# Performance work log

Measured on AMD Instinct MI355X. Metric: run time of the kernel, lower is better.

## Reference

```python
import jax, jax.numpy as jnp
import numpy as np

B, L, E, H = 8, 2048, 768, 512

def setup_inputs() -> dict:
    key = jax.random.key(0)
    ks = jax.random.split(key, 12)
    s = 0.05
    rn = lambda k, shp: jax.random.normal(k, shp, dtype=jnp.float32) * s
    return {
        "embedded_inputs": jax.random.normal(ks[0], (B, L, E), dtype=jnp.float32),
        "decoder_input_init": jax.random.normal(ks[1], (B, H), dtype=jnp.float32),
        "W_ih": rn(ks[2], (4 * H, E)), "W_hh": rn(ks[3], (4 * H, H)),
        "b_ih": jnp.zeros((4 * H,), jnp.float32), "b_hh": jnp.zeros((4 * H,), jnp.float32),
        "Wd_in": rn(ks[4], (4 * H, H)), "bd_in": jnp.zeros((4 * H,), jnp.float32),
        "Wd_hh": rn(ks[5], (4 * H, H)), "bd_hh": jnp.zeros((4 * H,), jnp.float32),
        "W_inp": rn(ks[6], (H, H)), "b_inp": jnp.zeros((H,), jnp.float32),
        "Wc": rn(ks[7], (H, H)), "bc": jnp.zeros((H,), jnp.float32),
        "V": jax.random.uniform(ks[8], (H,), minval=-1.0, maxval=1.0, dtype=jnp.float32),
        "W_out": rn(ks[9], (H, 2 * H)), "b_out": jnp.zeros((H,), jnp.float32),
    }


def _lstm_cell(x, h, c, W_in, b_in, W_hid, b_hid):
    # gates chunked in (input, forget, cell, out) order, matching torch .chunk(4,1)
    g = x @ W_in.T + b_in + h @ W_hid.T + b_hid
    i, f, gc, o = jnp.split(g, 4, axis=-1)
    c_t = jax.nn.sigmoid(f) * c + jax.nn.sigmoid(i) * jnp.tanh(gc)
    h_t = jax.nn.sigmoid(o) * jnp.tanh(c_t)
    return h_t, c_t


def _encode(x, W_ih, W_hh, b_ih, b_hh):
    # x: [B, L, E] -> outputs [B, L, H], last (h, c)
    Hh = W_hh.shape[1]
    h0 = jnp.zeros((x.shape[0], Hh), x.dtype)
    def step(carry, xt):
        h, c = carry
        h, c = _lstm_cell(xt, h, c, W_ih, b_ih, W_hh, b_hh)
        return (h, c), h
    (hT, cT), outs = jax.lax.scan(step, (h0, h0), x.transpose(1, 0, 2))
    return outs.transpose(1, 0, 2), hT, cT


def reference(embedded_inputs, decoder_input_init, W_ih, W_hh, b_ih, b_hh,
              Wd_in, bd_in, Wd_hh, bd_hh, W_inp, b_inp, Wc, bc, V, W_out, b_out):
    enc_out, h, c = _encode(embedded_inputs, W_ih, W_hh, b_ih, b_hh)  # [B,L,H]
    context = enc_out
    Bc, Lc = context.shape[0], context.shape[1]
    # Conv1d(k=1) over permuted context == per-position linear -> ctx [B,H,L]
    ctx = jnp.einsum('blh,oh->bol', context, Wc) + bc[None, :, None]
    mask = jnp.ones((Bc, Lc), context.dtype)
    x = decoder_input_init
    outputs, pointers = [], []
    for _ in range(2):  # source decodes exactly 2 pointers (start/end)
        h_t, c = _lstm_cell(x, h, c, Wd_in, bd_in, Wd_hh, bd_hh)
        inp = (h_t @ W_inp.T + b_inp)[:, :, None]                 # [B,H,1]
        att = jnp.einsum('h,bhl->bl', V, jnp.tanh(inp + ctx))     # [B,L]
        att = jnp.where(mask == 0, -jnp.inf, att)
        alpha = jax.nn.softmax(att, axis=1)
        hidden_state = jnp.einsum('bhl,bl->bh', ctx, alpha)
        h = jnp.tanh(jnp.concatenate([hidden_state, h_t], axis=-1) @ W_out.T + b_out)
        idx = jnp.argmax(alpha * mask, axis=1)
        onehot = jax.nn.one_hot(idx, Lc, dtype=mask.dtype)
        mask = mask * (1.0 - onehot)
        x = jnp.take_along_axis(enc_out, idx[:, None, None], axis=1)[:, 0, :]
        outputs.append(alpha)
        pointers.append(idx)
    return jnp.stack(outputs, axis=1), jnp.stack(pointers, axis=1)
```

## Files before the change

kernel.cpp:

```cpp
#include <hip/hip_runtime.h>
#include <math.h>

#define B_   8
#define L_   2048
#define E_   768
#define H_   512
#define G4_  2048
#define CL_  512

static __device__ __forceinline__ float sigm(float x){ return 1.0f/(1.0f+expf(-x)); }

__global__ __launch_bounds__(256) void gemm128(
    const float* __restrict__ A, const float* __restrict__ W,
    const float* __restrict__ bias1, const float* __restrict__ bias2,
    float* __restrict__ C, int M, int N, int K, int CL, int Ltot, int c0)
{
  __shared__ float As[16][132];
  __shared__ float Bs[16][132];
  const int tid = threadIdx.x;
  const int bm = blockIdx.y * 128, bn = blockIdx.x * 128;

  const int r  = tid >> 1;
  const int kq = (tid & 1) * 8;
  const int am = bm + r;
  const int ab = am / CL, al = am % CL;
  const float* Arow = A + ((size_t)ab * Ltot + c0 + al) * K;
  const float* Wrow = W + (size_t)(bn + r) * K;

  const int tx = tid & 15, ty = tid >> 4;
  float acc[8][8] = {};

  for (int k0 = 0; k0 < K; k0 += 16) {
    float4 a0 = *(const float4*)(Arow + k0 + kq);
    float4 a1 = *(const float4*)(Arow + k0 + kq + 4);
    float4 w0 = *(const float4*)(Wrow + k0 + kq);
    float4 w1 = *(const float4*)(Wrow + k0 + kq + 4);
    __syncthreads();
    As[kq+0][r]=a0.x; As[kq+1][r]=a0.y; As[kq+2][r]=a0.z; As[kq+3][r]=a0.w;
    As[kq+4][r]=a1.x; As[kq+5][r]=a1.y; As[kq+6][r]=a1.z; As[kq+7][r]=a1.w;
    Bs[kq+0][r]=w0.x; Bs[kq+1][r]=w0.y; Bs[kq+2][r]=w0.z; Bs[kq+3][r]=w0.w;
    Bs[kq+4][r]=w1.x; Bs[kq+5][r]=w1.y; Bs[kq+6][r]=w1.z; Bs[kq+7][r]=w1.w;
    __syncthreads();
    #pragma unroll
    for (int k = 0; k < 16; ++k) {
      float4 x0 = *(const float4*)&As[k][ty*4];
      float4 x1 = *(const float4*)&As[k][64 + ty*4];
      float4 y0 = *(const float4*)&Bs[k][tx*4];
      float4 y1 = *(const float4*)&Bs[k][64 + tx*4];
      float av[8] = {x0.x,x0.y,x0.z,x0.w, x1.x,x1.y,x1.z,x1.w};
      float bv[8] = {y0.x,y0.y,y0.z,y0.w, y1.x,y1.y,y1.z,y1.w};
      #pragma unroll
      for (int i=0;i<8;++i)
        #pragma unroll
        for (int j=0;j<8;++j)
          acc[i][j] += av[i]*bv[j];
    }
  }

  float bs[8];
  #pragma unroll
  for (int j=0;j<4;++j) {
    int c0n = bn + tx*4 + j, c1n = bn + 64 + tx*4 + j;
    bs[j]   = bias1[c0n] + (bias2 ? bias2[c0n] : 0.0f);
    bs[4+j] = bias1[c1n] + (bias2 ? bias2[c1n] : 0.0f);
  }
  #pragma unroll
  for (int i=0;i<8;++i) {
    int row = bm + ((i<4) ? (ty*4+i) : (64 + ty*4 + (i-4)));
    float4 o0 = { acc[i][0]+bs[0], acc[i][1]+bs[1], acc[i][2]+bs[2], acc[i][3]+bs[3] };
    float4 o1 = { acc[i][4]+bs[4], acc[i][5]+bs[5], acc[i][6]+bs[6], acc[i][7]+bs[7] };
    *(float4*)&C[(size_t)row*N + bn + tx*4]      = o0;
    *(float4*)&C[(size_t)row*N + bn + 64 + tx*4] = o1;
  }
}

__global__ __launch_bounds__(256, 1) void recur3(
    const float* __restrict__ Xp,
    const float* __restrict__ Whh,
    float* __restrict__ enc_out,
    unsigned long long* __restrict__ hb2,
    float* __restrict__ cbuf,
    float* __restrict__ hT,
    int t0, int nsteps)
{
  const int tid = threadIdx.x;
  const int b   = blockIdx.x & 7;
  const int m   = blockIdx.x >> 3;
  const int cq  = tid >> 4, q = tid & 15;
  const int gi_c = cq >> 2;
  const int jb   = (cq & 3) * 8;

  __shared__ float hsh[2][512];
  __shared__ float gsum[2][128];
  __shared__ float xpsh[2][128];

  float4 w4[8][8];
  #pragma unroll
  for (int r = 0; r < 8; ++r) {
    const float* wr = Whh + ((size_t)(gi_c*H_ + m*32 + jb + r))*H_ + q*4;
    #pragma unroll
    for (int k = 0; k < 8; ++k) w4[r][k] = *(const float4*)(wr + k*64);
  }
  float cc = 0.0f;
  if (tid < 32) cc = cbuf[b*H_ + m*32 + tid];

  const bool ownPoll = ((tid >> 4) == m);

  for (int s = 0; s < nsteps; ++s) {
    const int t = t0 + s;
    const int p = s & 1;

    float xv = 0.0f;
    if (tid < 128)
      xv = Xp[((size_t)(b*CL_ + s))*G4_ + (size_t)(tid>>5)*H_ + m*32 + (tid&31)];

    if (!(ownPoll && s > 0)) {
      const unsigned long long* src =
          hb2 + ((size_t)(t & 1))*(B_*H_) + (size_t)b*H_ + tid*2;
      unsigned long long v0 = 0, v1 = 0;
      bool d0 = false, d1 = false;
      do {
        if (!d0) v0 = __hip_atomic_load(src,   __ATOMIC_RELAXED, __HIP_MEMORY_SCOPE_AGENT);
        if (!d1) v1 = __hip_atomic_load(src+1, __ATOMIC_RELAXED, __HIP_MEMORY_SCOPE_AGENT);
        d0 = d0 || ((unsigned)(v0 >> 32) == (unsigned)t);
        d1 = d1 || ((unsigned)(v1 >> 32) == (unsigned)t);
      } while (!(d0 && d1));
      union { unsigned u; float f; } a0, a1;
      a0.u = (unsigned)v0; a1.u = (unsigned)v1;
      hsh[p][2*tid]   = a0.f;
      hsh[p][2*tid+1] = a1.f;
    }
    if (tid < 128) xpsh[p][tid] = xv;
    __syncthreads();

    float acc[8] = {0,0,0,0,0,0,0,0};
    #pragma unroll
    for (int k = 0; k < 8; ++k) {
      float4 h4 = *(const float4*)&hsh[p][q*4 + k*64];
      #pragma unroll
      for (int r = 0; r < 8; ++r) {
        acc[r] = fmaf(w4[r][k].x, h4.x, acc[r]);
        acc[r] = fmaf(w4[r][k].y, h4.y, acc[r]);
        acc[r] = fmaf(w4[r][k].z, h4.z, acc[r]);
        acc[r] = fmaf(w4[r][k].w, h4.w, acc[r]);
      }
    }
    #pragma unroll
    for (int msk = 1; msk < 16; msk <<= 1)
      #pragma unroll
      for (int r = 0; r < 8; ++r) acc[r] += __shfl_xor(acc[r], msk, 64);
    if (q < 8) gsum[p][cq*8 + q] = acc[q];
    __syncthreads();

    if (tid < 32) {
      float g0 = gsum[p][tid]      + xpsh[p][tid];
      float g1 = gsum[p][32 + tid] + xpsh[p][32 + tid];
      float g2 = gsum[p][64 + tid] + xpsh[p][64 + tid];
      float g3 = gsum[p][96 + tid] + xpsh[p][96 + tid];
      cc = sigm(g1)*cc + sigm(g0)*tanhf(g2);
      float hn = sigm(g3)*tanhf(cc);
      const int j = m*32 + tid;
      union { float f; unsigned u; } hu; hu.f = hn;
      unsigned long long wv =
          (((unsigned long long)(unsigned)(t + 1)) << 32) | (unsigned long long)hu.u;
      __hip_atomic_store(hb2 + ((size_t)((t+1) & 1))*(B_*H_) + (size_t)b*H_ + j, wv,
                         __ATOMIC_RELAXED, __HIP_MEMORY_SCOPE_AGENT);
      hsh[p^1][j] = hn;
      enc_out[((size_t)b*L_ + t)*H_ + j] = hn;
      if (t == L_ - 1) hT[b*H_ + j] = hn;
    }
  }
  if (tid < 32) cbuf[b*H_ + m*32 + tid] = cc;
}

__global__ __launch_bounds__(256) void dual_mv(
    const float* __restrict__ x1, const float* __restrict__ W1, int ld1, int K1,
    const float* __restrict__ x2, const float* __restrict__ W2, int ld2, int K2,
    const float* __restrict__ bias1, const float* __restrict__ bias2,
    float* __restrict__ out, int N, int act)
{
  const int w = blockIdx.x*4 + (threadIdx.x>>6);
  const int lane = threadIdx.x & 63;
  const int b = w / N, n = w % N;
  float s = 0.0f;
  for (int k = lane*4; k < K1; k += 256) {
    float4 xv = *(const float4*)(x1 + (size_t)b*K1 + k);
    float4 wv = *(const float4*)(W1 + (size_t)n*ld1 + k);
    s += xv.x*wv.x + xv.y*wv.y + xv.z*wv.z + xv.w*wv.w;
  }
  if (x2) {
    for (int k = lane*4; k < K2; k += 256) {
      float4 xv = *(const float4*)(x2 + (size_t)b*K2 + k);
      float4 wv = *(const float4*)(W2 + (size_t)n*ld2 + k);
      s += xv.x*wv.x + xv.y*wv.y + xv.z*wv.z + xv.w*wv.w;
    }
  }
  #pragma unroll
  for (int m=32; m>0; m>>=1) s += __shfl_xor(s, m, 64);
  if (lane == 0) {
    float r = s + bias1[n] + (bias2 ? bias2[n] : 0.0f);
    if (act) r = tanhf(r);
    out[(size_t)b*N + n] = r;
  }
}

__global__ void dec_cell(const float* __restrict__ g, float* __restrict__ c,
                         float* __restrict__ ht)
{
  int i = blockIdx.x*256 + threadIdx.x;
  int b = i >> 9, j = i & 511;
  const float* gb = g + (size_t)b*G4_;
  float gi_ = gb[j], gf = gb[H_+j], gg = gb[2*H_+j], go = gb[3*H_+j];
  float cc = c[i];
  cc = sigm(gf)*cc + sigm(gi_)*tanhf(gg);
  ht[i] = sigm(go)*tanhf(cc);
  c[i]  = cc;
}

__global__ __launch_bounds__(256) void dec_att(
    const float* __restrict__ inp, const float* __restrict__ ctx,
    const float* __restrict__ V, float* __restrict__ att)
{
  const int w = blockIdx.x*4 + (threadIdx.x>>6);
  const int lane = threadIdx.x & 63;
  const int b = w >> 11;
  const float* cr = ctx + (size_t)w*H_;
  const float* ip = inp + (size_t)b*H_;
  float s = 0.0f;
  #pragma unroll
  for (int i=0;i<2;++i) {
    int k = lane*4 + i*256;
    float4 c4 = *(const float4*)(cr+k);
    float4 i4 = *(const float4*)(ip+k);
    float4 v4 = *(const float4*)(V+k);
    s += v4.x*tanhf(i4.x+c4.x) + v4.y*tanhf(i4.y+c4.y)
       + v4.z*tanhf(i4.z+c4.z) + v4.w*tanhf(i4.w+c4.w);
  }
  #pragma unroll
  for (int m=32; m>0; m>>=1) s += __shfl_xor(s, m, 64);
  if (lane == 0) att[w] = s;
}

__global__ __launch_bounds__(256) void dec_softmax(
    const float* __restrict__ att, const float* __restrict__ enc,
    int iter, int* __restrict__ chosen,
    float* __restrict__ out_alpha, float* __restrict__ out_ptr,
    float* __restrict__ x_next)
{
  const int b = blockIdx.x, tid = threadIdx.x;
  __shared__ float rv[256]; __shared__ int ri[256];
  __shared__ float s_mx, s_sum; __shared__ int s_idx;
  const int banned = iter ? chosen[b] : -1;
  float a[8]; float mx = -INFINITY;
  #pragma unroll
  for (int i=0;i<8;++i) {
    int l = (i<<8)+tid;
    float v = att[(size_t)b*L_ + l];
    if (l == banned) v = -INFINITY;
    a[i] = v; mx = fmaxf(mx, v);
  }
  rv[tid]=mx; __syncthreads();
  for (int s=128;s>0;s>>=1){ if (tid<s) rv[tid]=fmaxf(rv[tid],rv[tid+s]); __syncthreads(); }
  if (tid==0) s_mx = rv[0];
  __syncthreads();
  const float MX = s_mx;
  __syncthreads();
  float sum = 0.0f;
  #pragma unroll
  for (int i=0;i<8;++i) {
    int l = (i<<8)+tid;
    float pexp = (l == banned) ? 0.0f : expf(a[i]-MX);
    sum += pexp; a[i] = pexp;
  }
  rv[tid]=sum; __syncthreads();
  for (int s=128;s>0;s>>=1){ if (tid<s) rv[tid]+=rv[tid+s]; __syncthreads(); }
  if (tid==0) s_sum = rv[0];
  __syncthreads();
  const float inv = 1.0f/s_sum;
  __syncthreads();
  float vb = -1.0f; int ib = 1<<30;
  #pragma unroll
  for (int i=0;i<8;++i) {
    int l = (i<<8)+tid;
    if (l != banned) { float v = a[i]; if (v > vb || (v == vb && l < ib)) { vb=v; ib=l; } }
  }
  rv[tid]=vb; ri[tid]=ib; __syncthreads();
  for (int s=128;s>0;s>>=1) {
    if (tid<s) {
      float v2=rv[tid+s]; int i2=ri[tid+s];
      if (v2 > rv[tid] || (v2 == rv[tid] && i2 < ri[tid])) { rv[tid]=v2; ri[tid]=i2; }
    }
    __syncthreads();
  }
  if (tid==0) {
    s_idx = ri[0];
    out_ptr[b*2+iter] = (float)ri[0];
    if (iter==0) chosen[b] = ri[0];
  }
  __syncthreads();
  #pragma unroll
  for (int i=0;i<8;++i) {
    int l = (i<<8)+tid;
    out_alpha[((size_t)b*2+iter)*L_ + l] = a[i]*inv;
  }
  const int idx = s_idx;
  for (int j=tid; j<H_; j+=256)
    x_next[(size_t)b*H_ + j] = enc[((size_t)b*L_ + idx)*H_ + j];
}

__global__ void dec_hidden1(const float* __restrict__ ctx, const float* __restrict__ alpha_all,
                            int iter, float* __restrict__ part)
{
  const int b = blockIdx.x >> 4, ch = blockIdx.x & 15;
  const int j = threadIdx.x;
  const float* al = alpha_all + ((size_t)b*2+iter)*L_ + ch*128;
  const float* cp = ctx + ((size_t)b*L_ + ch*128)*H_ + j;
  float s = 0.0f;
  for (int l=0; l<128; ++l) s += cp[(size_t)l*H_] * al[l];
  part[((size_t)b*16+ch)*H_ + j] = s;
}

__global__ void dec_hidden2(const float* __restrict__ part, float* __restrict__ hid)
{
  int i = blockIdx.x*256 + threadIdx.x;
  int b = i >> 9, j = i & 511;
  float s = 0.0f;
  #pragma unroll
  for (int ch=0; ch<16; ++ch) s += part[((size_t)b*16+ch)*H_ + j];
  hid[i] = s;
}

extern "C" void kernel_launch(void* const* d_in, const int* in_sizes, int n_in,
                              void* d_out, int out_size, void* d_ws, size_t ws_size,
                              hipStream_t stream)
{
  const float* emb   = (const float*)d_in[0];
  const float* x0    = (const float*)d_in[1];
  const float* W_ih  = (const float*)d_in[2];
  const float* W_hh  = (const float*)d_in[3];
  const float* b_ih  = (const float*)d_in[4];
  const float* b_hh  = (const float*)d_in[5];
  const float* Wd_in = (const float*)d_in[6];
  const float* bd_in = (const float*)d_in[7];
  const float* Wd_hh = (const float*)d_in[8];
  const float* bd_hh = (const float*)d_in[9];
  const float* W_inp = (const float*)d_in[10];
  const float* b_inp = (const float*)d_in[11];
  const float* Wc    = (const float*)d_in[12];
  const float* bc    = (const float*)d_in[13];
  const float* V     = (const float*)d_in[14];
  const float* W_out = (const float*)d_in[15];
  const float* b_out = (const float*)d_in[16];

  float* ws  = (float*)d_ws;
  float* XP  = ws;
  float* CTX = ws;
  float* ENC = XP + (size_t)8388608;
  unsigned long long* HB2 = (unsigned long long*)(ENC + (size_t)8388608);
  float* HB  = (float*)(HB2 + 8192);
  float* CB  = HB + 4096;
  float* DG  = CB + 4096;
  float* HT  = DG + 16384;
  float* INP = HT + 4096;
  float* ATT = INP + 4096;
  float* HID = ATT + 16384;
  float* XN  = HID + 4096;
  float* HD  = XN + 4096;
  float* PART = HD + 4096;
  int* CHOSEN = (int*)(PART + 65536);

  hipMemsetAsync(HB2, 0, 8192*sizeof(unsigned long long) + (4096+4096)*sizeof(float), stream);

  for (int c=0; c<4; ++c) {
    gemm128<<<dim3(G4_/128, (B_*CL_)/128), 256, 0, stream>>>(
        emb, W_ih, b_ih, b_hh, XP, B_*CL_, G4_, E_, CL_, L_, c*CL_);
    recur3<<<128, 256, 0, stream>>>(XP, W_hh, ENC, HB2, CB, HB, c*CL_, CL_);
  }
  gemm128<<<dim3(H_/128, (B_*L_)/128), 256, 0, stream>>>(
      ENC, Wc, bc, nullptr, CTX, B_*L_, H_, H_, L_, L_, 0);

  float* out = (float*)d_out;
  const float* x_cur = x0;
  const float* h_cur = HB;
  for (int iter=0; iter<2; ++iter) {
    dual_mv<<<(B_*G4_)/4, 256, 0, stream>>>(x_cur, Wd_in, H_, H_,
                                            h_cur, Wd_hh, H_, H_,
                                            bd_in, bd_hh, DG, G4_, 0);
    dec_cell<<<16, 256, 0, stream>>>(DG, CB, HT);
    dual_mv<<<(B_*H_)/4, 256, 0, stream>>>(HT, W_inp, H_, H_,
                                           nullptr, nullptr, 0, 0,
                                           b_inp, nullptr, INP, H_, 0);
    dec_att<<<(B_*L_)/4, 256, 0, stream>>>(INP, CTX, V, ATT);
    dec_softmax<<<B_, 256, 0, stream>>>(ATT, ENC, iter, CHOSEN, out, out + 32768, XN);
    dec_hidden1<<<B_*16, 512, 0, stream>>>(CTX, out, iter, PART);
    dec_hidden2<<<16, 256, 0, stream>>>(PART, HID);
    dual_mv<<<(B_*H_)/4, 256, 0, stream>>>(HID, W_out, 2*H_, H_,
                                           HT, W_out + H_, 2*H_, H_,
                                           b_out, nullptr, HD, H_, 1);
    x_cur = XN; h_cur = HD;
  }
}
```

Baseline: 5.740 ms.

## Split recurrent LSTM kernel over 256 blocks with 16 hidden units each

The persistent recurrent kernel now runs 256 blocks, each owning 16 hidden units per batch row instead of 32. Each 16-lane group computes all four gates for one unit, so the shared-memory gate sum and the second __syncthreads per step go away. The next step's input projection is prefetched a step early, and tanhf is replaced with an exp-based tanh. The costs are more blocks polling the global h buffer each step, a spin-wait that assumes all 256 blocks are resident at once, and small accuracy changes from the custom tanh.

```diff
diff --git a/kernel.cpp b/kernel.cpp
--- a/kernel.cpp
+++ b/kernel.cpp
@@ -9,6 +9,12 @@
 #define CL_  512
 
 static __device__ __forceinline__ float sigm(float x){ return 1.0f/(1.0f+expf(-x)); }
+static __device__ __forceinline__ float ftanh(float x){
+  float ax = fabsf(x);
+  float e  = expf(2.0f*ax);
+  float r  = 1.0f - 2.0f/(e+1.0f);
+  return copysignf(r, x);
+}
 
 __global__ __launch_bounds__(256) void gemm128(
     const float* __restrict__ A, const float* __restrict__ W,
@@ -74,7 +80,7 @@
   }
 }
 
-__global__ __launch_bounds__(256, 1) void recur3(
+__global__ __launch_bounds__(256, 1) void recur4(
     const float* __restrict__ Xp,
     const float* __restrict__ Whh,
     float* __restrict__ enc_out,
@@ -86,35 +92,40 @@
   const int tid = threadIdx.x;
   const int b   = blockIdx.x & 7;
   const int m   = blockIdx.x >> 3;
-  const int cq  = tid >> 4, q = tid & 15;
-  const int gi_c = cq >> 2;
-  const int jb   = (cq & 3) * 8;
+  const int c   = tid >> 4;
+  const int q   = tid & 15;
+  const int j   = m*16 + c;
 
   __shared__ float hsh[2][512];
-  __shared__ float gsum[2][128];
-  __shared__ float xpsh[2][128];
-
-  float4 w4[8][8];
-  #pragma unroll
-  for (int r = 0; r < 8; ++r) {
-    const float* wr = Whh + ((size_t)(gi_c*H_ + m*32 + jb + r))*H_ + q*4;
+  __shared__ float xpsh[2][64];
+
+  float4 w4[4][8];
+  #pragma unroll
+  for (int gi = 0; gi < 4; ++gi) {
+    const float* wr = Whh + ((size_t)(gi*H_ + j))*H_ + q*4;
     #pragma unroll
-    for (int k = 0; k < 8; ++k) w4[r][k] = *(const float4*)(wr + k*64);
+    for (int k = 0; k < 8; ++k) w4[gi][k] = *(const float4*)(wr + k*64);
   }
   float cc = 0.0f;
-  if (tid < 32) cc = cbuf[b*H_ + m*32 + tid];
-
-  const bool ownPoll = ((tid >> 4) == m);
+  if (q == 0) cc = cbuf[b*H_ + j];
+
+  float xv = 0.0f;
+  if (tid < 64)
+    xv = Xp[((size_t)(b*CL_ + 0))*G4_ + (size_t)(tid>>4)*H_ + m*16 + (tid&15)];
+
+  const bool own = ((tid >> 3) == m);
 
   for (int s = 0; s < nsteps; ++s) {
     const int t = t0 + s;
     const int p = s & 1;
 
-    float xv = 0.0f;
-    if (tid < 128)
-      xv = Xp[((size_t)(b*CL_ + s))*G4_ + (size_t)(tid>>5)*H_ + m*32 + (tid&31)];
-
-    if (!(ownPoll && s > 0)) {
+    if (tid < 64) {
+      xpsh[p][tid] = xv;
+      if (s + 1 < nsteps)
+        xv = Xp[((size_t)(b*CL_ + s + 1))*G4_ + (size_t)(tid>>4)*H_ + m*16 + (tid&15)];
+    }
+
+    if (!(own && s > 0)) {
       const unsigned long long* src =
           hb2 + ((size_t)(t & 1))*(B_*H_) + (size_t)b*H_ + tid*2;
       unsigned long long v0 = 0, v1 = 0;
@@ -130,36 +141,35 @@
       hsh[p][2*tid]   = a0.f;
       hsh[p][2*tid+1] = a1.f;
     }
-    if (tid < 128) xpsh[p][tid] = xv;
     __syncthreads();
 
-    float acc[8] = {0,0,0,0,0,0,0,0};
+    float xg0=0.f, xg1=0.f, xg2=0.f, xg3=0.f;
+    if (q == 0) {
+      xg0 = xpsh[p][c];      xg1 = xpsh[p][16+c];
+      xg2 = xpsh[p][32+c];   xg3 = xpsh[p][48+c];
+    }
+
+    float a0=0.f, a1=0.f, a2=0.f, a3=0.f;
     #pragma unroll
     for (int k = 0; k < 8; ++k) {
       float4 h4 = *(const float4*)&hsh[p][q*4 + k*64];
-      #pragma unroll
-      for (int r = 0; r < 8; ++r) {
-        acc[r] = fmaf(w4[r][k].x, h4.x, acc[r]);
-        acc[r] = fmaf(w4[r][k].y, h4.y, acc[r]);
-        acc[r] = fmaf(w4[r][k].z, h4.z, acc[r]);
-        acc[r] = fmaf(w4[r][k].w, h4.w, acc[r]);
-      }
+      a0 = fmaf(w4[0][k].x,h4.x, fmaf(w4[0][k].y,h4.y, fmaf(w4[0][k].z,h4.z, fmaf(w4[0][k].w,h4.w, a0))));
+      a1 = fmaf(w4[1][k].x,h4.x, fmaf(w4[1][k].y,h4.y, fmaf(w4[1][k].z,h4.z, fmaf(w4[1][k].w,h4.w, a1))));
+      a2 = fmaf(w4[2][k].x,h4.x, fmaf(w4[2][k].y,h4.y, fmaf(w4[2][k].z,h4.z, fmaf(w4[2][k].w,h4.w, a2))));
+      a3 = fmaf(w4[3][k].x,h4.x, fmaf(w4[3][k].y,h4.y, fmaf(w4[3][k].z,h4.z, fmaf(w4[3][k].w,h4.w, a3))));
     }
     #pragma unroll
-    for (int msk = 1; msk < 16; msk <<= 1)
-      #pragma unroll
-      for (int r = 0; r < 8; ++r) acc[r] += __shfl_xor(acc[r], msk, 64);
-    if (q < 8) gsum[p][cq*8 + q] = acc[q];
-    __syncthreads();
-
-    if (tid < 32) {
-      float g0 = gsum[p][tid]      + xpsh[p][tid];
-      float g1 = gsum[p][32 + tid] + xpsh[p][32 + tid];
-      float g2 = gsum[p][64 + tid] + xpsh[p][64 + tid];
-      float g3 = gsum[p][96 + tid] + xpsh[p][96 + tid];
-      cc = sigm(g1)*cc + sigm(g0)*tanhf(g2);
-      float hn = sigm(g3)*tanhf(cc);
-      const int j = m*32 + tid;
+    for (int msk = 1; msk < 16; msk <<= 1) {
+      a0 += __shfl_xor(a0, msk, 64);
+      a1 += __shfl_xor(a1, msk, 64);
+      a2 += __shfl_xor(a2, msk, 64);
+      a3 += __shfl_xor(a3, msk, 64);
+    }
+
+    if (q == 0) {
+      float g0 = a0 + xg0, g1 = a1 + xg1, g2 = a2 + xg2, g3 = a3 + xg3;
+      cc = sigm(g1)*cc + sigm(g0)*ftanh(g2);
+      float hn = sigm(g3)*ftanh(cc);
       union { float f; unsigned u; } hu; hu.f = hn;
       unsigned long long wv =
           (((unsigned long long)(unsigned)(t + 1)) << 32) | (unsigned long long)hu.u;
@@ -170,7 +180,7 @@
       if (t == L_ - 1) hT[b*H_ + j] = hn;
     }
   }
-  if (tid < 32) cbuf[b*H_ + m*32 + tid] = cc;
+  if (q == 0) cbuf[b*H_ + j] = cc;
 }
 
 __global__ __launch_bounds__(256) void dual_mv(
@@ -374,7 +384,7 @@
   for (int c=0; c<4; ++c) {
     gemm128<<<dim3(G4_/128, (B_*CL_)/128), 256, 0, stream>>>(
         emb, W_ih, b_ih, b_hh, XP, B_*CL_, G4_, E_, CL_, L_, c*CL_);
-    recur3<<<128, 256, 0, stream>>>(XP, W_hh, ENC, HB2, CB, HB, c*CL_, CL_);
+    recur4<<<256, 256, 0, stream>>>(XP, W_hh, ENC, HB2, CB, HB, c*CL_, CL_);
   }
   gemm128<<<dim3(H_/128, (B_*L_)/128), 256, 0, stream>>>(
       ENC, Wc, bc, nullptr, CTX, B_*L_, H_, H_, L_, L_, 0);
```

Result: slower. 7.009 ms (+22.1%).
